# Optimization experiments

Hardware: AMD Instinct MI355X
Metric: run time of the kernel (lower is better)

Reference implementation:

```python
import jax, jax.numpy as jnp
import numpy as np

K = 3
PAD = 1


def conv2d(x, w, b, pad):
    y = jax.lax.conv_general_dilated(
        x, w, window_strides=(1, 1), padding=[(pad, pad), (pad, pad)],
        dimension_numbers=("NCHW", "OIHW", "NCHW"))
    return y + b[None, :, None, None]


def dcn_v2(f, w_off, b_off, w, b):
    # Modulated deformable conv (DCNv2), stride=1, pad=1, dilation=1, dg=1.
    B, C, H, W = f.shape
    om = conv2d(f, w_off, b_off, PAD)                 # [B, 27, H, W]
    o1, o2, m = jnp.split(om, 3, axis=1)
    offset = jnp.concatenate([o1, o2], axis=1).reshape(B, K * K, 2, H, W)
    dy, dx = offset[:, :, 0], offset[:, :, 1]          # [B, 9, H, W]
    mask = jax.nn.sigmoid(m)                           # [B, 9, H, W]
    ky = (jnp.arange(K * K) // K).astype(f.dtype)      # kernel row per tap
    kx = (jnp.arange(K * K) % K).astype(f.dtype)       # kernel col per tap
    hh = jnp.arange(H, dtype=f.dtype)
    ww = jnp.arange(W, dtype=f.dtype)
    ys = hh[None, None, :, None] - PAD + ky[None, :, None, None] + dy  # [B,9,H,W]
    xs = ww[None, None, None, :] - PAD + kx[None, :, None, None] + dx
    y0 = jnp.floor(ys)
    x0 = jnp.floor(xs)
    wy1 = ys - y0
    wx1 = xs - x0
    wy0 = 1.0 - wy1
    wx0 = 1.0 - wx1
    f_flat = f.reshape(B, C, H * W)

    def gather(yi, xi):
        valid = (yi >= 0) & (yi <= H - 1) & (xi >= 0) & (xi <= W - 1)
        yc = jnp.clip(yi, 0, H - 1).astype(jnp.int32)
        xc = jnp.clip(xi, 0, W - 1).astype(jnp.int32)
        idx = (yc * W + xc).reshape(B, 1, -1)          # [B,1,9*H*W]
        g = jnp.take_along_axis(f_flat, idx, axis=2).reshape(B, C, K * K, H, W)
        return g * valid.astype(f.dtype).reshape(B, 1, K * K, H, W)

    v = (gather(y0, x0) * (wy0 * wx0)[:, None]
         + gather(y0, x0 + 1) * (wy0 * wx1)[:, None]
         + gather(y0 + 1, x0) * (wy1 * wx0)[:, None]
         + gather(y0 + 1, x0 + 1) * (wy1 * wx1)[:, None])   # [B,C,9,H,W]
    v = v * mask[:, None]
    out = jnp.einsum("bckhw,ock->bohw", v, w.reshape(w.shape[0], C, K * K))
    return out + b[None, :, None, None]


def setup_inputs() -> dict:
    key = jax.random.key(0)
    ks = jax.random.split(key, 10)
    B, C, H, W = 2, 256, 128, 128
    s = 0.05
    return {
        "x": jax.random.normal(ks[0], (B, C, H, W), jnp.float32),
        "votes": jax.random.normal(ks[1], (B, C, H, W), jnp.float32),
        "w1": jax.random.normal(ks[2], (C, C, 3, 3), jnp.float32) * s,
        "b1": jnp.zeros((C,), jnp.float32),
        "w_off": jax.random.normal(ks[3], (27, C, 3, 3), jnp.float32) * 0.01,
        "b_off": jnp.zeros((27,), jnp.float32),
        "w_dcn": jax.random.normal(ks[4], (C, C, 3, 3), jnp.float32) * s,
        "b_dcn": jnp.zeros((C,), jnp.float32),
        "w2": jax.random.normal(ks[5], (C, C, 3, 3), jnp.float32) * s,
        "b2": jnp.zeros((C,), jnp.float32),
        "w3": jax.random.normal(ks[6], (C, C, 3, 3), jnp.float32) * s,
        "b3": jnp.zeros((C,), jnp.float32),
        "w4": jax.random.normal(ks[7], (2, C, 1, 1), jnp.float32) * s,
        "b4": jnp.zeros((2,), jnp.float32),
    }


def reference(x, votes, w1, b1, w_off, b_off, w_dcn, b_dcn, w2, b2, w3, b3, w4, b4):
    v = jax.nn.relu(votes)
    t = jax.nn.relu(conv2d(v, w1, b1, PAD))            # conv3x3 + relu
    t = jax.nn.relu(dcn_v2(t, w_off, b_off, w_dcn, b_dcn))  # DCN + relu
    t = conv2d(t, w2, b2, PAD)                         # conv3x3 (no relu)
    g = t * x                                          # gated by x
    h = jax.nn.relu(conv2d(g, w3, b3, PAD))            # conv3x3 + relu
    out = conv2d(h, w4, b4, 0)                         # 1x1 -> outplanes
    return out
```

## Files before the change

### kernel.cpp

```cpp
#include <hip/hip_runtime.h>
#include <math.h>

typedef short short8 __attribute__((ext_vector_type(8)));
typedef float f32x4 __attribute__((ext_vector_type(4)));
typedef unsigned int uint4v __attribute__((ext_vector_type(4)));
typedef unsigned short ushort_t;

__device__ inline ushort_t f2bf(float f) {
    unsigned u = __builtin_bit_cast(unsigned, f);
    u = (u + 0x7fffu + ((u >> 16) & 1u)) >> 16;
    return (ushort_t)u;
}
__device__ inline float bf2f(ushort_t u) {
    return __builtin_bit_cast(float, (unsigned)u << 16);
}
__device__ inline void gload_lds16(const ushort_t* g, short* l) {
    __builtin_amdgcn_global_load_lds((const __attribute__((address_space(1))) unsigned int*)g,
                                     (__attribute__((address_space(3))) unsigned int*)l, 16, 0, 0);
}

__device__ inline void wpack_body(const float* __restrict__ w, ushort_t* __restrict__ wpk,
                                  int COUT, int NF, int bidLocal, int tid) {
    int T = bidLocal * 256 + tid;
    int lane = T & 63;
    int rest = T >> 6;
    int n = rest % NF;
    int kstep = rest / NF;
    int t = kstep >> 3, cc = kstep & 7;
    int oc = n * 16 + (lane & 15);
    int kk = (lane >> 4) * 8;
    short8 sv;
#pragma unroll
    for (int j = 0; j < 8; ++j) {
        int ci = cc * 32 + kk + j;
        float val = (oc < COUT) ? w[((size_t)oc * 256 + ci) * 9 + t] : 0.f;
        sv[j] = (short)f2bf(val);
    }
    *(short8*)&wpk[(size_t)T * 8] = sv;
}

__global__ __launch_bounds__(256)
void wpack_all_kernel(const float* w1, ushort_t* wpk1,
                      const float* w_off, ushort_t* wpkO,
                      const float* w_dcn, ushort_t* wpkD,
                      const float* w2, ushort_t* wpk2,
                      const float* w3, ushort_t* wpk3,
                      ushort_t* zp) {
    int bid = blockIdx.x, tid = threadIdx.x;
    if (bid < 288)       wpack_body(w1,    wpk1, 256, 16, bid,        tid);
    else if (bid < 324)  wpack_body(w_off, wpkO, 27,  2,  bid - 288,  tid);
    else if (bid < 612)  wpack_body(w_dcn, wpkD, 256, 16, bid - 324,  tid);
    else if (bid < 900)  wpack_body(w2,    wpk2, 256, 16, bid - 612,  tid);
    else if (bid < 1188) wpack_body(w3,    wpk3, 256, 16, bid - 900,  tid);
    else                 zp[tid] = 0;
}

__global__ __launch_bounds__(256)
void nhwc_all_kernel(const float* __restrict__ votes, const float* __restrict__ x,
                     ushort_t* __restrict__ aN, ushort_t* __restrict__ xN) {
    __shared__ short s[64 * 66];
    const int tid = threadIdx.x;
    const int px0 = blockIdx.x * 64;
    const int ci0 = blockIdx.y * 64;
    const int z   = blockIdx.z;
    const int b   = z & 1;
    const bool doRelu = (z < 2);
    const float* inb = (doRelu ? votes : x) + (size_t)b * 256 * 16384;
    ushort_t* ob = (doRelu ? aN : xN) + (size_t)b * 16384 * 256;
#pragma unroll
    for (int rep = 0; rep < 16; ++rep) {
        int cl = rep * 4 + (tid >> 6);
        int pl = tid & 63;
        float v = inb[(size_t)(ci0 + cl) * 16384 + px0 + pl];
        if (doRelu) v = fmaxf(v, 0.f);
        s[pl * 66 + cl] = (short)f2bf(v);
    }
    __syncthreads();
#pragma unroll
    for (int rep = 0; rep < 2; ++rep) {
        int c = rep * 256 + tid;
        int pl = c >> 3;
        int cl = (c & 7) * 8;
        *(short8*)&ob[(size_t)(px0 + pl) * 256 + ci0 + cl] = *(const short8*)&s[pl * 66 + cl];
    }
}

template<int TW, int OUTC, int EPI>
__global__ __launch_bounds__(512, 2)
void conv_mfma_kernel(const ushort_t* __restrict__ in, const ushort_t* __restrict__ wpk,
                      const float* __restrict__ bias, int coutReal,
                      const ushort_t* __restrict__ xin, ushort_t* __restrict__ outp,
                      const ushort_t* __restrict__ zp,
                      const float* __restrict__ w4g, const float* __restrict__ b4g,
                      float* __restrict__ out4)
{
    constexpr int NF = OUTC / 16;
    constexpr int NN = (NF < 4) ? NF : 4;
    constexpr int HWD = TW + 2;
    constexpr int HPX = 6 * HWD;
    constexpr int ROUNDS = (HPX * 4 + 511) / 512;
    constexpr int MW  = TW / 16;
    constexpr int MPW = TW / 8;
    constexpr int PITCH = OUTC + 4;
    union SM { short a[2][ROUNDS * 512 * 8]; float e[TW * PITCH]; };
    __shared__ __align__(16) SM sm;

    const int tid  = threadIdx.x;
    const int lane = tid & 63;
    const int wv   = tid >> 6;
    const int hi   = lane >> 4;
    const int lo   = lane & 15;
    const int pxg  = wv & 1;
    const int wn   = wv >> 1;
    const int wnu  = __builtin_amdgcn_readfirstlane(wn);
    const int x0 = blockIdx.x * TW;
    const int y0 = blockIdx.y * 4;
    const int b  = blockIdx.z;
    const ushort_t* inb = in + (size_t)b * 16384 * 256;

    const ushort_t* sptr[ROUNDS];
    int sstep[ROUNDS];
#pragma unroll
    for (int r = 0; r < ROUNDS; ++r) {
        int g = r * 512 + tid;
        int px = g >> 2, slot = g & 3;
        int hy = px / HWD, hx = px - hy * HWD;
        int gy = y0 - 1 + hy, gx = x0 - 1 + hx;
        bool ok = (px < HPX) && ((unsigned)gy < 128u) && ((unsigned)gx < 128u);
        int kk = (px ^ (px >> 2)) & 3;
        sptr[r] = ok ? (inb + (size_t)((gy << 7) + gx) * 256 + ((slot ^ kk) << 3))
                     : (zp + (slot << 3));
        sstep[r] = ok ? 32 : 0;
    }

    int pxh_base[MPW];
#pragma unroll
    for (int m = 0; m < MPW; ++m)
        pxh_base[m] = (2 * pxg + m / MW) * HWD + (m % MW) * 16 + lo;

    f32x4 acc[MPW][NN];
#pragma unroll
    for (int m = 0; m < MPW; ++m)
#pragma unroll
        for (int n = 0; n < NN; ++n) acc[m][n] = (f32x4){0.f, 0.f, 0.f, 0.f};

#pragma unroll
    for (int r = 0; r < ROUNDS; ++r)
        gload_lds16(sptr[r], &sm.a[0][(r * 512 + wv * 64) * 8]);
    __syncthreads();

    for (int cc = 0; cc < 8; ++cc) {
        const int buf = cc & 1;
        if (cc < 7) {
#pragma unroll
            for (int r = 0; r < ROUNDS; ++r)
                gload_lds16(sptr[r] + (size_t)(cc + 1) * sstep[r],
                            &sm.a[buf ^ 1][(r * 512 + wv * 64) * 8]);
        }
        if (NF >= 4 || wnu == 0) {
#pragma unroll
            for (int t = 0; t < 9; ++t) {
                const int ky = t / 3, kx = t % 3;
                short8 bf[NN];
#pragma unroll
                for (int n = 0; n < NN; ++n)
                    bf[n] = *(const short8*)&wpk[((size_t)((t * 8 + cc) * NF + wnu * NN + n) * 64 + lane) * 8];
                short8 af[MPW];
#pragma unroll
                for (int m = 0; m < MPW; ++m) {
                    int ph = pxh_base[m] + ky * HWD + kx;
                    int off = ph * 32 + ((hi ^ ((ph ^ (ph >> 2)) & 3)) << 3);
                    af[m] = *(const short8*)&sm.a[buf][off];
                }
#pragma unroll
                for (int m = 0; m < MPW; ++m)
#pragma unroll
                    for (int n = 0; n < NN; ++n)
                        acc[m][n] = __builtin_amdgcn_mfma_f32_16x16x32_bf16(af[m], bf[n], acc[m][n], 0, 0, 0);
            }
        }
        __syncthreads();
    }

    float br[NN];
#pragma unroll
    for (int n = 0; n < NN; ++n) {
        int oc = wn * (16 * NN) + n * 16 + lo;
        br[n] = (oc < coutReal) ? bias[oc] : 0.f;
    }
    const size_t obase = ((size_t)b * 16384 + (size_t)y0 * 128 + x0) * OUTC;
#pragma unroll
    for (int p = 0; p < 4; ++p) {
        if (pxg == (p >> 1) && (NF >= 4 || wnu == 0)) {
#pragma unroll
            for (int mm = 0; mm < MW; ++mm) {
                int m = (p & 1) * MW + mm;
#pragma unroll
                for (int n = 0; n < NN; ++n)
#pragma unroll
                    for (int r = 0; r < 4; ++r) {
                        int col = mm * 16 + hi * 4 + r;
                        float v = acc[m][n][r] + br[n];
                        if (EPI == 1 || EPI == 3) v = fmaxf(v, 0.f);
                        sm.e[col * PITCH + wn * (16 * NN) + n * 16 + lo] = v;
                    }
            }
        }
        __syncthreads();
        if constexpr (EPI == 3) {
            int col = tid >> 5;
            int ch  = tid & 31;
            f32x4 v0 = *(const f32x4*)&sm.e[col * PITCH + ch * 8];
            f32x4 v1 = *(const f32x4*)&sm.e[col * PITCH + ch * 8 + 4];
            float4 wa0 = *(const float4*)&w4g[ch * 8];
            float4 wa1 = *(const float4*)&w4g[ch * 8 + 4];
            float4 wb0 = *(const float4*)&w4g[256 + ch * 8];
            float4 wb1 = *(const float4*)&w4g[256 + ch * 8 + 4];
            float a0 = v0[0] * wa0.x + v0[1] * wa0.y + v0[2] * wa0.z + v0[3] * wa0.w
                     + v1[0] * wa1.x + v1[1] * wa1.y + v1[2] * wa1.z + v1[3] * wa1.w;
            float a1 = v0[0] * wb0.x + v0[1] * wb0.y + v0[2] * wb0.z + v0[3] * wb0.w
                     + v1[0] * wb1.x + v1[1] * wb1.y + v1[2] * wb1.z + v1[3] * wb1.w;
#pragma unroll
            for (int s = 16; s >= 1; s >>= 1) {
                a0 += __shfl_xor(a0, s);
                a1 += __shfl_xor(a1, s);
            }
            if (ch == 0) {
                size_t o = (size_t)b * 2 * 16384 + (size_t)(y0 + p) * 128 + x0 + col;
                out4[o]         = a0 + b4g[0];
                out4[o + 16384] = a1 + b4g[1];
            }
        } else {
            constexpr int CHUNKS = TW * OUTC / 8;
            for (int c = tid; c < CHUNKS; c += 512) {
                int col = c / (OUTC / 8);
                int ch = c % (OUTC / 8);
                f32x4 v0 = *(const f32x4*)&sm.e[col * PITCH + ch * 8];
                f32x4 v1 = *(const f32x4*)&sm.e[col * PITCH + ch * 8 + 4];
                size_t gidx = obase + ((size_t)p * 128 + col) * OUTC + ch * 8;
                if (EPI == 2) {
                    uint4v xu = *(const uint4v*)&xin[gidx];
#pragma unroll
                    for (int j = 0; j < 4; ++j) {
                        float xa = bf2f((ushort_t)(xu[j] & 0xffffu));
                        float xb = __builtin_bit_cast(float, xu[j] & 0xffff0000u);
                        if (j < 2) { v0[2 * j] *= xa; v0[2 * j + 1] *= xb; }
                        else       { v1[2 * (j - 2)] *= xa; v1[2 * (j - 2) + 1] *= xb; }
                    }
                }
                short8 s;
#pragma unroll
                for (int j = 0; j < 4; ++j) s[j] = (short)f2bf(v0[j]);
#pragma unroll
                for (int j = 0; j < 4; ++j) s[4 + j] = (short)f2bf(v1[j]);
                *(short8*)&outp[gidx] = s;
            }
        }
        __syncthreads();
    }
}

__device__ inline void corner8(uint4v u, float w, float* sv) {
#pragma unroll
    for (int j = 0; j < 4; ++j) {
        unsigned a = u[j];
        sv[2 * j]     = fmaf(w, __builtin_bit_cast(float, a << 16), sv[2 * j]);
        sv[2 * j + 1] = fmaf(w, __builtin_bit_cast(float, a & 0xffff0000u), sv[2 * j + 1]);
    }
}

__global__ __launch_bounds__(256, 2)
void dcn_mfma_kernel(const ushort_t* __restrict__ ft, const ushort_t* __restrict__ omt,
                     const ushort_t* __restrict__ wpk, const float* __restrict__ bias,
                     ushort_t* __restrict__ outp)
{
    union SM { short a[2][2][2048]; float e[16 * 264]; };
    __shared__ __align__(16) SM sm;

    const int tid  = threadIdx.x;
    const int lane = tid & 63;
    const int wv   = tid >> 6;
    const int hi   = lane >> 4;
    const int lo   = lane & 15;
    const int bid  = blockIdx.x;
    const int tile = (bid & 7) * 64 + (bid >> 3);
    const int b    = tile >> 8;
    const int rem  = tile & 255;
    const int y0   = (rem >> 3) * 4;
    const int x0   = (rem & 7) * 16;
    const ushort_t* fb = ft + (size_t)b * 16384 * 256;

    const int pxl = (wv << 4) | (lane >> 2);
    const int q   = lane & 3;

    float mw[9][4];
    unsigned mc[9];
    {
        const int py = y0 + (pxl >> 4), pxx = x0 + (pxl & 15);
        const ushort_t* omp = omt + ((size_t)b * 16384 + py * 128 + pxx) * 32;
        uint4v ow[4];
#pragma unroll
        for (int j = 0; j < 4; ++j) ow[j] = *(const uint4v*)(omp + j * 8);
        unsigned wbuf[14];
#pragma unroll
        for (int j = 0; j < 4; ++j)
#pragma unroll
            for (int e = 0; e < 4; ++e)
                if (j * 4 + e < 14) wbuf[j * 4 + e] = ow[j][e];
#pragma unroll
        for (int t = 0; t < 9; ++t) {
            float dy = bf2f((ushort_t)(wbuf[t] & 0xffffu));
            float dx = bf2f((ushort_t)(wbuf[t] >> 16));
            unsigned mw_ = wbuf[(18 + t) >> 1];
            float mr = ((18 + t) & 1) ? bf2f((ushort_t)(mw_ >> 16)) : bf2f((ushort_t)(mw_ & 0xffffu));
            float mk = 1.f / (1.f + expf(-mr));
            float ys = (float)(py - 1 + t / 3) + dy;
            float xs = (float)(pxx - 1 + t % 3) + dx;
            float y0f = floorf(ys), x0f = floorf(xs);
            float wy1 = ys - y0f, wx1 = xs - x0f;
            float wy0 = 1.f - wy1, wx0 = 1.f - wx1;
            int yi = (int)y0f, xi = (int)x0f;
            bool vy0 = (yi >= 0) && (yi < 128), vy1 = (yi + 1 >= 0) && (yi + 1 < 128);
            bool vx0 = (xi >= 0) && (xi < 128), vx1 = (xi + 1 >= 0) && (xi + 1 < 128);
            mw[t][0] = (vy0 && vx0) ? wy0 * wx0 * mk : 0.f;
            mw[t][1] = (vy0 && vx1) ? wy0 * wx1 * mk : 0.f;
            mw[t][2] = (vy1 && vx0) ? wy1 * wx0 * mk : 0.f;
            mw[t][3] = (vy1 && vx1) ? wy1 * wx1 * mk : 0.f;
            int y0c = min(max(yi, 0), 127), y1c = min(max(yi + 1, 0), 127);
            int x0c = min(max(xi, 0), 127), x1c = min(max(xi + 1, 0), 127);
            mc[t] = (unsigned)y0c | ((unsigned)y1c << 8) | ((unsigned)x0c << 16) | ((unsigned)x1c << 24);
        }
    }

    const int w_off = pxl * 32 + ((q ^ ((pxl ^ (pxl >> 2)) & 3)) << 3);
    int a_off[4];
#pragma unroll
    for (int m = 0; m < 4; ++m) {
        int p_ = m * 16 + lo;
        a_off[m] = p_ * 32 + ((hi ^ ((p_ ^ (p_ >> 2)) & 3)) << 3);
    }

    f32x4 acc[4][4];
#pragma unroll
    for (int m = 0; m < 4; ++m)
#pragma unroll
        for (int n = 0; n < 4; ++n) acc[m][n] = (f32x4){0.f, 0.f, 0.f, 0.f};

    uint4v n0a, n0b, n0c, n0d;
    uint4v n1a, n1b, n1c, n1d;

    {
        unsigned c = mc[0];
        int yy0 = c & 255, yy1 = (c >> 8) & 255, xx0 = (c >> 16) & 255, xx1 = c >> 24;
        size_t o00 = (size_t)((yy0 << 7) + xx0) * 256, o01 = (size_t)((yy0 << 7) + xx1) * 256;
        size_t o10 = (size_t)((yy1 << 7) + xx0) * 256, o11 = (size_t)((yy1 << 7) + xx1) * 256;
#pragma unroll
        for (int h = 0; h < 2; ++h) {
            const ushort_t* pc = fb + h * 32 + q * 8;
            uint4v g0 = *(const uint4v*)(pc + o00);
            uint4v g1 = *(const uint4v*)(pc + o01);
            uint4v g2 = *(const uint4v*)(pc + o10);
            uint4v g3 = *(const uint4v*)(pc + o11);
            float sv[8] = {0.f, 0.f, 0.f, 0.f, 0.f, 0.f, 0.f, 0.f};
            corner8(g0, mw[0][0], sv); corner8(g1, mw[0][1], sv);
            corner8(g2, mw[0][2], sv); corner8(g3, mw[0][3], sv);
            unsigned pk[4];
#pragma unroll
            for (int j = 0; j < 4; ++j)
                asm("v_cvt_pk_bf16_f32 %0, %1, %2" : "=v"(pk[j]) : "v"(sv[2 * j]), "v"(sv[2 * j + 1]));
            *(uint4v*)&sm.a[0][h][w_off] = (uint4v){pk[0], pk[1], pk[2], pk[3]};
        }
    }
    __syncthreads();

    for (int cch = 0; cch < 4; ++cch) {
#pragma unroll
        for (int t = 0; t < 9; ++t) {
            const int cur = (cch + t) & 1;
            const bool last = (cch == 3) && (t == 8);
            const int tn   = (t == 8) ? 0 : t + 1;
            const int cchn = (t == 8) ? cch + 1 : cch;
            if (!last) {
                unsigned c = mc[tn];
                int yy0 = c & 255, yy1 = (c >> 8) & 255, xx0 = (c >> 16) & 255, xx1 = c >> 24;
                size_t o00 = (size_t)((yy0 << 7) + xx0) * 256, o01 = (size_t)((yy0 << 7) + xx1) * 256;
                size_t o10 = (size_t)((yy1 << 7) + xx0) * 256, o11 = (size_t)((yy1 << 7) + xx1) * 256;
                const ushort_t* pc0 = fb + (2 * cchn) * 32 + q * 8;
                n0a = *(const uint4v*)(pc0 + o00);
                n0b = *(const uint4v*)(pc0 + o01);
                n0c = *(const uint4v*)(pc0 + o10);
                n0d = *(const uint4v*)(pc0 + o11);
                const ushort_t* pc1 = pc0 + 32;
                n1a = *(const uint4v*)(pc1 + o00);
                n1b = *(const uint4v*)(pc1 + o01);
                n1c = *(const uint4v*)(pc1 + o10);
                n1d = *(const uint4v*)(pc1 + o11);
            }
            short8 bfr0[4], bfr1[4];
            {
                const ushort_t* bs0 = wpk + ((size_t)((t * 8 + 2 * cch) * 16 + wv * 4) * 64 + lane) * 8;
#pragma unroll
                for (int n = 0; n < 4; ++n)
                    bfr0[n] = *(const short8*)(bs0 + (size_t)n * 512);
                const ushort_t* bs1 = bs0 + 16 * 512;
#pragma unroll
                for (int n = 0; n < 4; ++n)
                    bfr1[n] = *(const short8*)(bs1 + (size_t)n * 512);
            }
#pragma unroll
            for (int m = 0; m < 4; ++m) {
                short8 af0 = *(const short8*)&sm.a[cur][0][a_off[m]];
                short8 af1 = *(const short8*)&sm.a[cur][1][a_off[m]];
#pragma unroll
                for (int n = 0; n < 4; ++n)
                    acc[m][n] = __builtin_amdgcn_mfma_f32_16x16x32_bf16(af0, bfr0[n], acc[m][n], 0, 0, 0);
#pragma unroll
                for (int n = 0; n < 4; ++n)
                    acc[m][n] = __builtin_amdgcn_mfma_f32_16x16x32_bf16(af1, bfr1[n], acc[m][n], 0, 0, 0);
            }
            if (!last) {
                {
                    float sv[8] = {0.f, 0.f, 0.f, 0.f, 0.f, 0.f, 0.f, 0.f};
                    corner8(n0a, mw[tn][0], sv); corner8(n0b, mw[tn][1], sv);
                    corner8(n0c, mw[tn][2], sv); corner8(n0d, mw[tn][3], sv);
                    unsigned pk[4];
#pragma unroll
                    for (int j = 0; j < 4; ++j)
                        asm("v_cvt_pk_bf16_f32 %0, %1, %2" : "=v"(pk[j]) : "v"(sv[2 * j]), "v"(sv[2 * j + 1]));
                    *(uint4v*)&sm.a[cur ^ 1][0][w_off] = (uint4v){pk[0], pk[1], pk[2], pk[3]};
                }
                {
                    float sv[8] = {0.f, 0.f, 0.f, 0.f, 0.f, 0.f, 0.f, 0.f};
                    corner8(n1a, mw[tn][0], sv); corner8(n1b, mw[tn][1], sv);
                    corner8(n1c, mw[tn][2], sv); corner8(n1d, mw[tn][3], sv);
                    unsigned pk[4];
#pragma unroll
                    for (int j = 0; j < 4; ++j)
                        asm("v_cvt_pk_bf16_f32 %0, %1, %2" : "=v"(pk[j]) : "v"(sv[2 * j]), "v"(sv[2 * j + 1]));
                    *(uint4v*)&sm.a[cur ^ 1][1][w_off] = (uint4v){pk[0], pk[1], pk[2], pk[3]};
                }
            }
            __syncthreads();
        }
    }

    float br[4];
#pragma unroll
    for (int n = 0; n < 4; ++n) br[n] = bias[wv * 64 + n * 16 + lo];
#pragma unroll
    for (int p = 0; p < 4; ++p) {
#pragma unroll
        for (int n = 0; n < 4; ++n)
#pragma unroll
            for (int r = 0; r < 4; ++r)
                sm.e[(hi * 4 + r) * 264 + wv * 64 + n * 16 + lo] = fmaxf(acc[p][n][r] + br[n], 0.f);
        __syncthreads();
#pragma unroll
        for (int j = 0; j < 2; ++j) {
            int c2 = j * 256 + tid;
            int pl = c2 >> 5, ch = c2 & 31;
            f32x4 v0 = *(const f32x4*)&sm.e[pl * 264 + ch * 8];
            f32x4 v1 = *(const f32x4*)&sm.e[pl * 264 + ch * 8 + 4];
            short8 s;
#pragma unroll
            for (int jj = 0; jj < 4; ++jj) s[jj] = (short)f2bf(v0[jj]);
#pragma unroll
            for (int jj = 0; jj < 4; ++jj) s[4 + jj] = (short)f2bf(v1[jj]);
            *(short8*)&outp[((size_t)b * 16384 + (size_t)(y0 + p) * 128 + x0 + pl) * 256 + ch * 8] = s;
        }
        __syncthreads();
    }
}

extern "C" void kernel_launch(void* const* d_in, const int* in_sizes, int n_in,
                              void* d_out, int out_size, void* d_ws, size_t ws_size,
                              hipStream_t stream) {
    const float* x     = (const float*)d_in[0];
    const float* votes = (const float*)d_in[1];
    const float* w1    = (const float*)d_in[2];
    const float* b1    = (const float*)d_in[3];
    const float* w_off = (const float*)d_in[4];
    const float* b_off = (const float*)d_in[5];
    const float* w_dcn = (const float*)d_in[6];
    const float* b_dcn = (const float*)d_in[7];
    const float* w2    = (const float*)d_in[8];
    const float* b2    = (const float*)d_in[9];
    const float* w3    = (const float*)d_in[10];
    const float* b3    = (const float*)d_in[11];
    const float* w4    = (const float*)d_in[12];
    const float* b4    = (const float*)d_in[13];
    float* outp = (float*)d_out;

    const int B = 2;
    const size_t featN = (size_t)B * 16384 * 256;

    ushort_t* ws   = (ushort_t*)d_ws;
    ushort_t* t1   = ws;
    ushort_t* t2   = t1 + featN;
    ushort_t* aN   = t2 + featN;
    ushort_t* xN   = aN + featN;
    ushort_t* om   = xN + featN;
    ushort_t* wpk1 = om + (size_t)B * 16384 * 32;
    ushort_t* wpkO = wpk1 + 589824;
    ushort_t* wpkD = wpkO + 73728;
    ushort_t* wpk2 = wpkD + 589824;
    ushort_t* wpk3 = wpk2 + 589824;
    ushort_t* zp   = wpk3 + 589824;

    wpack_all_kernel<<<1189, 256, 0, stream>>>(w1, wpk1, w_off, wpkO, w_dcn, wpkD,
                                               w2, wpk2, w3, wpk3, zp);
    nhwc_all_kernel<<<dim3(256, 4, 4), 256, 0, stream>>>(votes, x, aN, xN);

    dim3 cg16(8, 32, B);
    conv_mfma_kernel<16, 256, 1><<<cg16, 512, 0, stream>>>(aN, wpk1, b1, 256, nullptr, t1, zp, nullptr, nullptr, nullptr);
    conv_mfma_kernel<16, 32, 0><<<cg16, 512, 0, stream>>>(t1, wpkO, b_off, 27, nullptr, om, zp, nullptr, nullptr, nullptr);
    dcn_mfma_kernel<<<512, 256, 0, stream>>>(t1, om, wpkD, b_dcn, t2);
    conv_mfma_kernel<16, 256, 2><<<cg16, 512, 0, stream>>>(t2, wpk2, b2, 256, xN, aN, zp, nullptr, nullptr, nullptr);
    conv_mfma_kernel<16, 256, 3><<<cg16, 512, 0, stream>>>(aN, wpk3, b3, 256, nullptr, nullptr, zp, w4, b4, outp);
}
```

Before: 244.5 us.

## Merge prep kernels and remap DCN gather lanes to 64-channel contiguous loads

Merges the weight-packing and NHWC-conversion kernels into one launch, removing a kernel launch and its gap. In the DCN kernel each thread now handles two pixels with 8 lanes per pixel covering 64 contiguous channels, instead of one pixel with 4 lanes reading two separate 32-channel halves. This is meant to make the bilinear corner gathers more contiguous (128 bytes per pixel corner) and better coalesced. The cost is twice the per-thread offset and mask metadata (mw, mc arrays), which raises register pressure and may lower occupancy or cause spills.

```diff
diff --git a/kernel.cpp b/kernel.cpp
--- a/kernel.cpp
+++ b/kernel.cpp
@@ -40,29 +40,26 @@
 }
 
 __global__ __launch_bounds__(256)
-void wpack_all_kernel(const float* w1, ushort_t* wpk1,
-                      const float* w_off, ushort_t* wpkO,
-                      const float* w_dcn, ushort_t* wpkD,
-                      const float* w2, ushort_t* wpk2,
-                      const float* w3, ushort_t* wpk3,
-                      ushort_t* zp) {
-    int bid = blockIdx.x, tid = threadIdx.x;
-    if (bid < 288)       wpack_body(w1,    wpk1, 256, 16, bid,        tid);
-    else if (bid < 324)  wpack_body(w_off, wpkO, 27,  2,  bid - 288,  tid);
-    else if (bid < 612)  wpack_body(w_dcn, wpkD, 256, 16, bid - 324,  tid);
-    else if (bid < 900)  wpack_body(w2,    wpk2, 256, 16, bid - 612,  tid);
-    else if (bid < 1188) wpack_body(w3,    wpk3, 256, 16, bid - 900,  tid);
-    else                 zp[tid] = 0;
-}
-
-__global__ __launch_bounds__(256)
-void nhwc_all_kernel(const float* __restrict__ votes, const float* __restrict__ x,
+void prep_all_kernel(const float* w1, ushort_t* wpk1,
+                     const float* w_off, ushort_t* wpkO,
+                     const float* w_dcn, ushort_t* wpkD,
+                     const float* w2, ushort_t* wpk2,
+                     const float* w3, ushort_t* wpk3,
+                     ushort_t* zp,
+                     const float* __restrict__ votes, const float* __restrict__ x,
                      ushort_t* __restrict__ aN, ushort_t* __restrict__ xN) {
     __shared__ short s[64 * 66];
-    const int tid = threadIdx.x;
-    const int px0 = blockIdx.x * 64;
-    const int ci0 = blockIdx.y * 64;
-    const int z   = blockIdx.z;
+    int bid = blockIdx.x, tid = threadIdx.x;
+    if (bid < 288)       { wpack_body(w1,    wpk1, 256, 16, bid,        tid); return; }
+    else if (bid < 324)  { wpack_body(w_off, wpkO, 27,  2,  bid - 288,  tid); return; }
+    else if (bid < 612)  { wpack_body(w_dcn, wpkD, 256, 16, bid - 324,  tid); return; }
+    else if (bid < 900)  { wpack_body(w2,    wpk2, 256, 16, bid - 612,  tid); return; }
+    else if (bid < 1188) { wpack_body(w3,    wpk3, 256, 16, bid - 900,  tid); return; }
+    else if (bid == 1188) { zp[tid] = 0; return; }
+    int nb = bid - 1189;
+    const int px0 = (nb & 255) * 64;
+    const int ci0 = ((nb >> 8) & 3) * 64;
+    const int z   = nb >> 10;
     const int b   = z & 1;
     const bool doRelu = (z < 2);
     const float* inb = (doRelu ? votes : x) + (size_t)b * 256 * 16384;
@@ -269,6 +266,42 @@
     }
 }
 
+__device__ inline void dcn_meta(const ushort_t* __restrict__ omp, int py, int pxx,
+                                float (&mw)[9][4], unsigned (&mc)[9]) {
+    uint4v ow[4];
+#pragma unroll
+    for (int j = 0; j < 4; ++j) ow[j] = *(const uint4v*)(omp + j * 8);
+    unsigned wbuf[14];
+#pragma unroll
+    for (int j = 0; j < 4; ++j)
+#pragma unroll
+        for (int e = 0; e < 4; ++e)
+            if (j * 4 + e < 14) wbuf[j * 4 + e] = ow[j][e];
+#pragma unroll
+    for (int t = 0; t < 9; ++t) {
+        float dy = bf2f((ushort_t)(wbuf[t] & 0xffffu));
+        float dx = bf2f((ushort_t)(wbuf[t] >> 16));
+        unsigned mw_ = wbuf[(18 + t) >> 1];
+        float mr = ((18 + t) & 1) ? bf2f((ushort_t)(mw_ >> 16)) : bf2f((ushort_t)(mw_ & 0xffffu));
+        float mk = 1.f / (1.f + expf(-mr));
+        float ys = (float)(py - 1 + t / 3) + dy;
+        float xs = (float)(pxx - 1 + t % 3) + dx;
+        float y0f = floorf(ys), x0f = floorf(xs);
+        float wy1 = ys - y0f, wx1 = xs - x0f;
+        float wy0 = 1.f - wy1, wx0 = 1.f - wx1;
+        int yi = (int)y0f, xi = (int)x0f;
+        bool vy0 = (yi >= 0) && (yi < 128), vy1 = (yi + 1 >= 0) && (yi + 1 < 128);
+        bool vx0 = (xi >= 0) && (xi < 128), vx1 = (xi + 1 >= 0) && (xi + 1 < 128);
+        mw[t][0] = (vy0 && vx0) ? wy0 * wx0 * mk : 0.f;
+        mw[t][1] = (vy0 && vx1) ? wy0 * wx1 * mk : 0.f;
+        mw[t][2] = (vy1 && vx0) ? wy1 * wx0 * mk : 0.f;
+        mw[t][3] = (vy1 && vx1) ? wy1 * wx1 * mk : 0.f;
+        int y0c = min(max(yi, 0), 127), y1c = min(max(yi + 1, 0), 127);
+        int x0c = min(max(xi, 0), 127), x1c = min(max(xi + 1, 0), 127);
+        mc[t] = (unsigned)y0c | ((unsigned)y1c << 8) | ((unsigned)x0c << 16) | ((unsigned)x1c << 24);
+    }
+}
+
 __global__ __launch_bounds__(256, 2)
 void dcn_mfma_kernel(const ushort_t* __restrict__ ft, const ushort_t* __restrict__ omt,
                      const ushort_t* __restrict__ wpk, const float* __restrict__ bias,
@@ -290,49 +323,23 @@
     const int x0   = (rem & 7) * 16;
     const ushort_t* fb = ft + (size_t)b * 16384 * 256;
 
-    const int pxl = (wv << 4) | (lane >> 2);
-    const int q   = lane & 3;
-
-    float mw[9][4];
-    unsigned mc[9];
+    const int px8 = lane >> 3;
+    const int q8  = lane & 7;
+    const int pxA = (wv << 4) | px8;
+    const int pxB = pxA + 8;
+    const int hA  = q8 >> 2;
+    const int qA  = q8 & 3;
+
+    float mwA[9][4], mwB[9][4];
+    unsigned mcA[9], mcB[9];
     {
-        const int py = y0 + (pxl >> 4), pxx = x0 + (pxl & 15);
-        const ushort_t* omp = omt + ((size_t)b * 16384 + py * 128 + pxx) * 32;
-        uint4v ow[4];
-#pragma unroll
-        for (int j = 0; j < 4; ++j) ow[j] = *(const uint4v*)(omp + j * 8);
-        unsigned wbuf[14];
-#pragma unroll
-        for (int j = 0; j < 4; ++j)
-#pragma unroll
-            for (int e = 0; e < 4; ++e)
-                if (j * 4 + e < 14) wbuf[j * 4 + e] = ow[j][e];
-#pragma unroll
-        for (int t = 0; t < 9; ++t) {
-            float dy = bf2f((ushort_t)(wbuf[t] & 0xffffu));
-            float dx = bf2f((ushort_t)(wbuf[t] >> 16));
-            unsigned mw_ = wbuf[(18 + t) >> 1];
-            float mr = ((18 + t) & 1) ? bf2f((ushort_t)(mw_ >> 16)) : bf2f((ushort_t)(mw_ & 0xffffu));
-            float mk = 1.f / (1.f + expf(-mr));
-            float ys = (float)(py - 1 + t / 3) + dy;
-            float xs = (float)(pxx - 1 + t % 3) + dx;
-            float y0f = floorf(ys), x0f = floorf(xs);
-            float wy1 = ys - y0f, wx1 = xs - x0f;
-            float wy0 = 1.f - wy1, wx0 = 1.f - wx1;
-            int yi = (int)y0f, xi = (int)x0f;
-            bool vy0 = (yi >= 0) && (yi < 128), vy1 = (yi + 1 >= 0) && (yi + 1 < 128);
-            bool vx0 = (xi >= 0) && (xi < 128), vx1 = (xi + 1 >= 0) && (xi + 1 < 128);
-            mw[t][0] = (vy0 && vx0) ? wy0 * wx0 * mk : 0.f;
-            mw[t][1] = (vy0 && vx1) ? wy0 * wx1 * mk : 0.f;
-            mw[t][2] = (vy1 && vx0) ? wy1 * wx0 * mk : 0.f;
-            mw[t][3] = (vy1 && vx1) ? wy1 * wx1 * mk : 0.f;
-            int y0c = min(max(yi, 0), 127), y1c = min(max(yi + 1, 0), 127);
-            int x0c = min(max(xi, 0), 127), x1c = min(max(xi + 1, 0), 127);
-            mc[t] = (unsigned)y0c | ((unsigned)y1c << 8) | ((unsigned)x0c << 16) | ((unsigned)x1c << 24);
-        }
-    }
-
-    const int w_off = pxl * 32 + ((q ^ ((pxl ^ (pxl >> 2)) & 3)) << 3);
+        const int py = y0 + wv;
+        dcn_meta(omt + ((size_t)b * 16384 + py * 128 + (x0 + px8)) * 32,     py, x0 + px8,     mwA, mcA);
+        dcn_meta(omt + ((size_t)b * 16384 + py * 128 + (x0 + px8 + 8)) * 32, py, x0 + px8 + 8, mwB, mcB);
+    }
+
+    const int wA = pxA * 32 + ((qA ^ ((pxA ^ (pxA >> 2)) & 3)) << 3);
+    const int wB = pxB * 32 + ((qA ^ ((pxB ^ (pxB >> 2)) & 3)) << 3);
     int a_off[4];
 #pragma unroll
     for (int m = 0; m < 4; ++m) {
@@ -346,31 +353,32 @@
 #pragma unroll
         for (int n = 0; n < 4; ++n) acc[m][n] = (f32x4){0.f, 0.f, 0.f, 0.f};
 
-    uint4v n0a, n0b, n0c, n0d;
-    uint4v n1a, n1b, n1c, n1d;
-
-    {
-        unsigned c = mc[0];
-        int yy0 = c & 255, yy1 = (c >> 8) & 255, xx0 = (c >> 16) & 255, xx1 = c >> 24;
-        size_t o00 = (size_t)((yy0 << 7) + xx0) * 256, o01 = (size_t)((yy0 << 7) + xx1) * 256;
-        size_t o10 = (size_t)((yy1 << 7) + xx0) * 256, o11 = (size_t)((yy1 << 7) + xx1) * 256;
-#pragma unroll
-        for (int h = 0; h < 2; ++h) {
-            const ushort_t* pc = fb + h * 32 + q * 8;
-            uint4v g0 = *(const uint4v*)(pc + o00);
-            uint4v g1 = *(const uint4v*)(pc + o01);
-            uint4v g2 = *(const uint4v*)(pc + o10);
-            uint4v g3 = *(const uint4v*)(pc + o11);
-            float sv[8] = {0.f, 0.f, 0.f, 0.f, 0.f, 0.f, 0.f, 0.f};
-            corner8(g0, mw[0][0], sv); corner8(g1, mw[0][1], sv);
-            corner8(g2, mw[0][2], sv); corner8(g3, mw[0][3], sv);
-            unsigned pk[4];
-#pragma unroll
-            for (int j = 0; j < 4; ++j)
-                asm("v_cvt_pk_bf16_f32 %0, %1, %2" : "=v"(pk[j]) : "v"(sv[2 * j]), "v"(sv[2 * j + 1]));
-            *(uint4v*)&sm.a[0][h][w_off] = (uint4v){pk[0], pk[1], pk[2], pk[3]};
-        }
-    }
+    uint4v nA0, nA1, nA2, nA3;
+    uint4v nB0, nB1, nB2, nB3;
+
+#define DCN_GATHER(NM0, NM1, NM2, NM3, MC, CCH_) { \
+    unsigned c = MC; \
+    int yy0 = c & 255, yy1 = (c >> 8) & 255, xx0 = (c >> 16) & 255, xx1 = c >> 24; \
+    const ushort_t* pc = fb + (CCH_) * 64 + q8 * 8; \
+    NM0 = *(const uint4v*)(pc + (size_t)((yy0 << 7) + xx0) * 256); \
+    NM1 = *(const uint4v*)(pc + (size_t)((yy0 << 7) + xx1) * 256); \
+    NM2 = *(const uint4v*)(pc + (size_t)((yy1 << 7) + xx0) * 256); \
+    NM3 = *(const uint4v*)(pc + (size_t)((yy1 << 7) + xx1) * 256); }
+
+#define DCN_COMBINE(NM0, NM1, NM2, NM3, MW, T_, WOFF, BUF) { \
+    float sv[8] = {0.f, 0.f, 0.f, 0.f, 0.f, 0.f, 0.f, 0.f}; \
+    corner8(NM0, MW[T_][0], sv); corner8(NM1, MW[T_][1], sv); \
+    corner8(NM2, MW[T_][2], sv); corner8(NM3, MW[T_][3], sv); \
+    unsigned pk[4]; \
+    _Pragma("unroll") \
+    for (int j = 0; j < 4; ++j) \
+        asm("v_cvt_pk_bf16_f32 %0, %1, %2" : "=v"(pk[j]) : "v"(sv[2 * j]), "v"(sv[2 * j + 1])); \
+    *(uint4v*)&sm.a[BUF][hA][WOFF] = (uint4v){pk[0], pk[1], pk[2], pk[3]}; }
+
+    DCN_GATHER(nA0, nA1, nA2, nA3, mcA[0], 0);
+    DCN_GATHER(nB0, nB1, nB2, nB3, mcB[0], 0);
+    DCN_COMBINE(nA0, nA1, nA2, nA3, mwA, 0, wA, 0);
+    DCN_COMBINE(nB0, nB1, nB2, nB3, mwB, 0, wB, 0);
     __syncthreads();
 
     for (int cch = 0; cch < 4; ++cch) {
@@ -381,20 +389,8 @@
             const int tn   = (t == 8) ? 0 : t + 1;
             const int cchn = (t == 8) ? cch + 1 : cch;
             if (!last) {
-                unsigned c = mc[tn];
-                int yy0 = c & 255, yy1 = (c >> 8) & 255, xx0 = (c >> 16) & 255, xx1 = c >> 24;
-                size_t o00 = (size_t)((yy0 << 7) + xx0) * 256, o01 = (size_t)((yy0 << 7) + xx1) * 256;
-                size_t o10 = (size_t)((yy1 << 7) + xx0) * 256, o11 = (size_t)((yy1 << 7) + xx1) * 256;
-                const ushort_t* pc0 = fb + (2 * cchn) * 32 + q * 8;
-                n0a = *(const uint4v*)(pc0 + o00);
-                n0b = *(const uint4v*)(pc0 + o01);
-                n0c = *(const uint4v*)(pc0 + o10);
-                n0d = *(const uint4v*)(pc0 + o11);
-                const ushort_t* pc1 = pc0 + 32;
-                n1a = *(const uint4v*)(pc1 + o00);
-                n1b = *(const uint4v*)(pc1 + o01);
-                n1c = *(const uint4v*)(pc1 + o10);
-                n1d = *(const uint4v*)(pc1 + o11);
+                DCN_GATHER(nA0, nA1, nA2, nA3, mcA[tn], cchn);
+                DCN_GATHER(nB0, nB1, nB2, nB3, mcB[tn], cchn);
             }
             short8 bfr0[4], bfr1[4];
             {
@@ -419,26 +415,8 @@
                     acc[m][n] = __builtin_amdgcn_mfma_f32_16x16x32_bf16(af1, bfr1[n], acc[m][n], 0, 0, 0);
             }
             if (!last) {
-                {
-                    float sv[8] = {0.f, 0.f, 0.f, 0.f, 0.f, 0.f, 0.f, 0.f};
-                    corner8(n0a, mw[tn][0], sv); corner8(n0b, mw[tn][1], sv);
-                    corner8(n0c, mw[tn][2], sv); corner8(n0d, mw[tn][3], sv);
-                    unsigned pk[4];
-#pragma unroll
-                    for (int j = 0; j < 4; ++j)
-                        asm("v_cvt_pk_bf16_f32 %0, %1, %2" : "=v"(pk[j]) : "v"(sv[2 * j]), "v"(sv[2 * j + 1]));
-                    *(uint4v*)&sm.a[cur ^ 1][0][w_off] = (uint4v){pk[0], pk[1], pk[2], pk[3]};
-                }
-                {
-                    float sv[8] = {0.f, 0.f, 0.f, 0.f, 0.f, 0.f, 0.f, 0.f};
-                    corner8(n1a, mw[tn][0], sv); corner8(n1b, mw[tn][1], sv);
-                    corner8(n1c, mw[tn][2], sv); corner8(n1d, mw[tn][3], sv);
-                    unsigned pk[4];
-#pragma unroll
-                    for (int j = 0; j < 4; ++j)
-                        asm("v_cvt_pk_bf16_f32 %0, %1, %2" : "=v"(pk[j]) : "v"(sv[2 * j]), "v"(sv[2 * j + 1]));
-                    *(uint4v*)&sm.a[cur ^ 1][1][w_off] = (uint4v){pk[0], pk[1], pk[2], pk[3]};
-                }
+                DCN_COMBINE(nA0, nA1, nA2, nA3, mwA, tn, wA, cur ^ 1);
+                DCN_COMBINE(nB0, nB1, nB2, nB3, mwB, tn, wB, cur ^ 1);
             }
             __syncthreads();
         }
@@ -507,9 +485,8 @@
     ushort_t* wpk3 = wpk2 + 589824;
     ushort_t* zp   = wpk3 + 589824;
 
-    wpack_all_kernel<<<1189, 256, 0, stream>>>(w1, wpk1, w_off, wpkO, w_dcn, wpkD,
-                                               w2, wpk2, w3, wpk3, zp);
-    nhwc_all_kernel<<<dim3(256, 4, 4), 256, 0, stream>>>(votes, x, aN, xN);
+    prep_all_kernel<<<1189 + 4096, 256, 0, stream>>>(w1, wpk1, w_off, wpkO, w_dcn, wpkD,
+                                                     w2, wpk2, w3, wpk3, zp, votes, x, aN, xN);
 
     dim3 cg16(8, 32, B);
     conv_mfma_kernel<16, 256, 1><<<cg16, 512, 0, stream>>>(aN, wpk1, b1, 256, nullptr, t1, zp, nullptr, nullptr, nullptr);
```

Result: slower. 317.1 us (+29.7%).
